# Kernel tuning notes

Measured on AMD Instinct MI355X. Metric: run time of the kernel, lower is better.

Reference implementation:

```python
import jax, jax.numpy as jnp
import numpy as np

BETA = 0.5

def setup_inputs() -> dict:
    key = jax.random.key(0)
    ks = jax.random.split(key, 12)
    B, H, d, hid = 2048, 100, 128, 256
    item_num, region_num, dist_num = 100000, 1000, 16
    return {
        "history": jax.random.randint(ks[0], (B, H), 0, item_num),
        "target": jax.random.randint(ks[1], (B,), 0, item_num),
        "history_region": jax.random.randint(ks[2], (B, H), 0, region_num),
        "target_region": jax.random.randint(ks[3], (B,), 0, region_num),
        "target_distance": jax.random.uniform(ks[4], (B,), dtype=jnp.float32),
        "E_hist": jax.random.normal(ks[5], (item_num, d), dtype=jnp.float32) * 0.01,
        "E_tgt": jax.random.normal(ks[6], (item_num, d), dtype=jnp.float32) * 0.01,
        "E_reg": jax.random.normal(ks[7], (region_num, d), dtype=jnp.float32) * 0.01,
        "E_dist": jax.random.normal(ks[8], (dist_num, d), dtype=jnp.float32) * 0.01,
        "W1": jax.random.normal(ks[9], (hid, 2 * d), dtype=jnp.float32) * 0.05,
        "b1": jnp.zeros((hid,), dtype=jnp.float32),
        "w2": jax.random.normal(ks[10], (hid,), dtype=jnp.float32) * 0.05,
    }

def reference(history, target, history_region, target_region, target_distance,
              E_hist, E_tgt, E_reg, E_dist, W1, b1, w2):
    # history embeddings: [B,H,2d]
    hist = jnp.concatenate([E_hist[history], E_reg[history_region]], axis=-1)
    # target embeddings: [B,1,2d]
    tgt = jnp.concatenate([E_tgt[target], E_reg[target_region]], axis=-1)[:, None, :]
    x = hist * tgt                                   # [B,H,2d]
    a = jax.nn.relu(jnp.einsum('bhd,kd->bhk', x, W1) + b1)  # [B,H,hid]
    score = jnp.einsum('bhk,k->bh', a, w2)           # [B,H]
    # distance bias: scalar per batch element
    dist = jnp.sum(target_distance[:, None] * E_dist[0], axis=1)  # [B]
    exp_A = jnp.exp(score + dist[:, None])           # [B,H]
    mask = (history != target[:, None]).astype(exp_A.dtype)
    exp_A = exp_A * mask
    exp_sum = jnp.power(jnp.sum(exp_A, axis=-1), BETA)  # [B]
    attn = exp_A / exp_sum[:, None]                  # [B,H]
    # weighted inner product: sum_h sum_d attn*hist*tgt
    pred = jnp.sum(hist * attn[:, :, None] * tgt, axis=(1, 2))  # [B]
    return jax.nn.sigmoid(pred)
```

## Files before the change

### kernel.cpp

```cpp
#include <hip/hip_runtime.h>
#include <stdint.h>

typedef __attribute__((ext_vector_type(8))) short bf16x8;
typedef __attribute__((ext_vector_type(4))) float f32x4;

#define HH  100
#define DD  128
#define HID 256

__device__ __forceinline__ unsigned short f2bf(float f) {
    unsigned int u = __float_as_uint(f);
    u += 0x7fffu + ((u >> 16) & 1u);
    return (unsigned short)(u >> 16);
}

__device__ __forceinline__ void load_lds_1k(const void* g, void* l) {
    __builtin_amdgcn_global_load_lds((const __attribute__((address_space(1))) unsigned int*)g,
                                     (__attribute__((address_space(3))) unsigned int*)l,
                                     16, 0, 0);
}

__global__ void w1_pack(const float* __restrict__ W1, unsigned short* __restrict__ W1p) {
    int unit = blockIdx.x * 256 + threadIdx.x;
    int lane = unit & 63;
    int s    = (unit >> 6) & 7;
    int st   = unit >> 9;
    int col  = lane & 15, quad = lane >> 4;
    const float* src = W1 + (size_t)(st * 16 + col) * HID + s * 32 + quad * 8;
    union { unsigned short u[8]; bf16x8 v; } o;
    #pragma unroll
    for (int j = 0; j < 8; j++) o.u[j] = f2bf(src[j]);
    *(bf16x8*)(W1p + (size_t)unit * 8) = o.v;
}

__global__ __launch_bounds__(512, 4) void nais_kernel(
    const int* __restrict__ history,
    const int* __restrict__ target,
    const int* __restrict__ history_region,
    const int* __restrict__ target_region,
    const float* __restrict__ target_distance,
    const float* __restrict__ E_hist,
    const float* __restrict__ E_tgt,
    const float* __restrict__ E_reg,
    const float* __restrict__ E_dist,
    const float* __restrict__ b1,
    const float* __restrict__ w2,
    const unsigned short* __restrict__ W1p,
    float* __restrict__ out)
{
    __shared__ __align__(16) unsigned short Bs[2][8192];
    __shared__ __align__(16) float tgts[HID];
    __shared__ __align__(16) float b1s[HID];
    __shared__ __align__(16) float w2s[HID];
    __shared__ float score[128];
    __shared__ float xsum[128];
    __shared__ float eA[HH];
    __shared__ float exs[HH];
    __shared__ int hidx[HH];
    __shared__ int hreg[HH];
    __shared__ float s_sumE;

    const int b    = blockIdx.x;
    const int t    = threadIdx.x;
    const int lane = t & 63;
    const int wave = t >> 6;
    const int col  = lane & 15;
    const int quad = lane >> 4;

    const int   tg    = target[b];
    const float tdist = target_distance[b];

    if (t < HH) {
        hidx[t] = history[b * HH + t];
        hreg[t] = history_region[b * HH + t];
    }
    if (wave == 4) {
        float4 v;
        if (lane < 32) v = *(const float4*)(E_tgt + (size_t)tg * DD + lane * 4);
        else           v = *(const float4*)(E_reg + (size_t)target_region[b] * DD + (lane - 32) * 4);
        *(float4*)(tgts + lane * 4) = v;
    }
    if (wave == 5) {
        *(float4*)(b1s + lane * 4) = *(const float4*)(b1 + lane * 4);
        *(float4*)(w2s + lane * 4) = *(const float4*)(w2 + lane * 4);
    }
    if (wave == 6) {
        float v = E_dist[lane] + E_dist[64 + lane];
        #pragma unroll
        for (int off = 32; off; off >>= 1) v += __shfl_xor(v, off);
        if (lane == 0) s_sumE = v;
    }
    __syncthreads();

    {
        const char* g = (const char*)W1p + wave * 2048 + lane * 16;
        char*       l = (char*)&Bs[0][0] + wave * 2048;
        load_lds_1k(g, l);
        load_lds_1k(g + 1024, l + 1024);
    }

    const int row = wave * 16 + col;
    const int rc  = (row < HH) ? row : row - 64;
    const int ih  = hidx[rc];
    const int ir  = hreg[rc];
    const float* ph = E_hist + (size_t)ih * DD + quad * 8;
    const float* pr = E_reg  + (size_t)ir * DD + quad * 8;
    bf16x8 afrag[8];
    float acc = 0.f;
    #pragma unroll
    for (int c = 0; c < 2; c++) {
        #pragma unroll
        for (int si = 0; si < 4; si++) {
            const int s = c * 4 + si;
            const float* src = (s < 4) ? (ph + s * 32) : (pr + (s - 4) * 32);
            float4 v0 = *(const float4*)src;
            float4 v1 = *(const float4*)(src + 4);
            const float* tp = tgts + s * 32 + quad * 8;
            float4 t0 = *(const float4*)tp, t1 = *(const float4*)(tp + 4);
            float x0 = v0.x * t0.x, x1 = v0.y * t0.y, x2 = v0.z * t0.z, x3 = v0.w * t0.w;
            float x4 = v1.x * t1.x, x5 = v1.y * t1.y, x6 = v1.z * t1.z, x7 = v1.w * t1.w;
            acc += (x0 + x1) + (x2 + x3) + ((x4 + x5) + (x6 + x7));
            union { unsigned short u[8]; bf16x8 v; } fb;
            fb.u[0] = f2bf(x0); fb.u[1] = f2bf(x1); fb.u[2] = f2bf(x2); fb.u[3] = f2bf(x3);
            fb.u[4] = f2bf(x4); fb.u[5] = f2bf(x5); fb.u[6] = f2bf(x6); fb.u[7] = f2bf(x7);
            afrag[s] = fb.v;
        }
        asm volatile("" ::: "memory");
    }
    {
        float v = acc;
        v += __shfl_xor(v, 16);
        v += __shfl_xor(v, 32);
        if (quad == 0) xsum[row] = v;
    }

    float sacc[4] = {};
    #pragma unroll 1
    for (int k = 0; k < 8; k++) {
        __syncthreads();
        if (k < 7) {
            const char* g = (const char*)W1p + (k + 1) * 16384 + wave * 2048 + lane * 16;
            char*       l = (char*)&Bs[(k + 1) & 1][0] + wave * 2048;
            load_lds_1k(g, l);
            load_lds_1k(g + 1024, l + 1024);
        }
        const unsigned short* buf = &Bs[k & 1][0];
        #pragma unroll
        for (int sti = 0; sti < 2; sti++) {
            const int st = k * 2 + sti;
            const float bb = b1s[st * 16 + col];
            const float ww = w2s[st * 16 + col];
            f32x4 acc0 = {0.f, 0.f, 0.f, 0.f};
            #pragma unroll
            for (int s = 0; s < 8; s++) {
                bf16x8 bfrag = *(const bf16x8*)(buf + ((sti * 8 + s) * 64 + lane) * 8);
                acc0 = __builtin_amdgcn_mfma_f32_16x16x32_bf16(afrag[s], bfrag, acc0, 0, 0, 0);
            }
            #pragma unroll
            for (int r = 0; r < 4; r++) {
                float z = acc0[r] + bb;
                sacc[r] += (z > 0.f) ? z * ww : 0.f;
            }
        }
    }
    #pragma unroll
    for (int r = 0; r < 4; r++) {
        float z = sacc[r];
        z += __shfl_xor(z, 1);
        z += __shfl_xor(z, 2);
        z += __shfl_xor(z, 4);
        z += __shfl_xor(z, 8);
        sacc[r] = z;
    }
    if (col == 0) {
        #pragma unroll
        for (int r = 0; r < 4; r++)
            score[wave * 16 + quad * 4 + r] = sacc[r];
    }

    __syncthreads();

    const float dist = tdist * s_sumE;
    if (t < HH) {
        float e = (hidx[t] != tg) ? expf(score[t] + dist) : 0.f;
        eA[t]  = e;
        exs[t] = e * xsum[t];
    }
    __syncthreads();
    if (t < 64) {
        float s1 = eA[t]  + ((t + 64 < HH) ? eA[t + 64]  : 0.f);
        float s2 = exs[t] + ((t + 64 < HH) ? exs[t + 64] : 0.f);
        #pragma unroll
        for (int off = 32; off; off >>= 1) {
            s1 += __shfl_xor(s1, off);
            s2 += __shfl_xor(s2, off);
        }
        if (t == 0) {
            float pred = s2 / sqrtf(s1);
            out[b] = 1.f / (1.f + expf(-pred));
        }
    }
}

extern "C" void kernel_launch(void* const* d_in, const int* in_sizes, int n_in,
                              void* d_out, int out_size, void* d_ws, size_t ws_size,
                              hipStream_t stream) {
    const int*   history         = (const int*)d_in[0];
    const int*   target          = (const int*)d_in[1];
    const int*   history_region  = (const int*)d_in[2];
    const int*   target_region   = (const int*)d_in[3];
    const float* target_distance = (const float*)d_in[4];
    const float* E_hist          = (const float*)d_in[5];
    const float* E_tgt           = (const float*)d_in[6];
    const float* E_reg           = (const float*)d_in[7];
    const float* E_dist          = (const float*)d_in[8];
    const float* W1              = (const float*)d_in[9];
    const float* b1              = (const float*)d_in[10];
    const float* w2              = (const float*)d_in[11];

    unsigned short* W1p = (unsigned short*)d_ws;
    const int B = in_sizes[1];

    w1_pack<<<32, 256, 0, stream>>>(W1, W1p);
    nais_kernel<<<B, 512, 0, stream>>>(history, target, history_region, target_region,
                                       target_distance, E_hist, E_tgt, E_reg, E_dist,
                                       b1, w2, W1p, (float*)d_out);
}
```

Baseline: 192.6 us.

## Switch MFMA to 32x32x16 tiles with 4 waves per block

Replaces the 16x16x32 bf16 MFMA tiling (8 waves of 16 rows) with 32x32x16 MFMA (4 waves of 32 rows), repacking W1 to match the new B-fragment layout and halving the block to 256 threads. Each wave now holds 16 A fragments and a 16-wide accumulator, and does more work per LDS-loaded B fragment. The intent is fewer MFMA issues and fewer LDS reads per output, and less redundant padded-row work. In exchange each wave uses more registers and the launch-bounds occupancy target is lower.

After: 198.1 us. 1.03x slower.

```diff
diff --git a/kernel.cpp b/kernel.cpp
--- a/kernel.cpp
+++ b/kernel.cpp
@@ -2,7 +2,7 @@
 #include <stdint.h>
 
 typedef __attribute__((ext_vector_type(8))) short bf16x8;
-typedef __attribute__((ext_vector_type(4))) float f32x4;
+typedef __attribute__((ext_vector_type(16))) float f32x16;
 
 #define HH  100
 #define DD  128
@@ -23,17 +23,18 @@
 __global__ void w1_pack(const float* __restrict__ W1, unsigned short* __restrict__ W1p) {
     int unit = blockIdx.x * 256 + threadIdx.x;
     int lane = unit & 63;
-    int s    = (unit >> 6) & 7;
-    int st   = unit >> 9;
-    int col  = lane & 15, quad = lane >> 4;
-    const float* src = W1 + (size_t)(st * 16 + col) * HID + s * 32 + quad * 8;
+    int s    = (unit >> 6) & 15;
+    int st   = unit >> 10;
+    int n    = st * 32 + (lane & 31);
+    int k    = s * 16 + (lane >> 5) * 8;
+    const float* src = W1 + (size_t)n * HID + k;
     union { unsigned short u[8]; bf16x8 v; } o;
     #pragma unroll
     for (int j = 0; j < 8; j++) o.u[j] = f2bf(src[j]);
     *(bf16x8*)(W1p + (size_t)unit * 8) = o.v;
 }
 
-__global__ __launch_bounds__(512, 4) void nais_kernel(
+__global__ __launch_bounds__(256, 2) void nais_kernel(
     const int* __restrict__ history,
     const int* __restrict__ target,
     const int* __restrict__ history_region,
@@ -64,8 +65,8 @@
     const int t    = threadIdx.x;
     const int lane = t & 63;
     const int wave = t >> 6;
-    const int col  = lane & 15;
-    const int quad = lane >> 4;
+    const int m32  = lane & 31;
+    const int half = lane >> 5;
 
     const int   tg    = target[b];
     const float tdist = target_distance[b];
@@ -74,48 +75,48 @@
         hidx[t] = history[b * HH + t];
         hreg[t] = history_region[b * HH + t];
     }
-    if (wave == 4) {
+    if (wave == 1) {
+        float v = E_dist[lane] + E_dist[64 + lane];
+        #pragma unroll
+        for (int off = 32; off; off >>= 1) v += __shfl_xor(v, off);
+        if (lane == 0) s_sumE = v;
+    }
+    if (wave == 2) {
         float4 v;
         if (lane < 32) v = *(const float4*)(E_tgt + (size_t)tg * DD + lane * 4);
         else           v = *(const float4*)(E_reg + (size_t)target_region[b] * DD + (lane - 32) * 4);
         *(float4*)(tgts + lane * 4) = v;
     }
-    if (wave == 5) {
+    if (wave == 3) {
         *(float4*)(b1s + lane * 4) = *(const float4*)(b1 + lane * 4);
         *(float4*)(w2s + lane * 4) = *(const float4*)(w2 + lane * 4);
     }
-    if (wave == 6) {
-        float v = E_dist[lane] + E_dist[64 + lane];
-        #pragma unroll
-        for (int off = 32; off; off >>= 1) v += __shfl_xor(v, off);
-        if (lane == 0) s_sumE = v;
-    }
     __syncthreads();
 
     {
-        const char* g = (const char*)W1p + wave * 2048 + lane * 16;
-        char*       l = (char*)&Bs[0][0] + wave * 2048;
-        load_lds_1k(g, l);
-        load_lds_1k(g + 1024, l + 1024);
-    }
-
-    const int row = wave * 16 + col;
+        const char* g = (const char*)W1p + wave * 4096 + lane * 16;
+        char*       l = (char*)&Bs[0][0] + wave * 4096;
+        #pragma unroll
+        for (int i = 0; i < 4; i++) load_lds_1k(g + i * 1024, l + i * 1024);
+    }
+
+    const int row = wave * 32 + m32;
     const int rc  = (row < HH) ? row : row - 64;
     const int ih  = hidx[rc];
     const int ir  = hreg[rc];
-    const float* ph = E_hist + (size_t)ih * DD + quad * 8;
-    const float* pr = E_reg  + (size_t)ir * DD + quad * 8;
-    bf16x8 afrag[8];
+    const float* ph = E_hist + (size_t)ih * DD + half * 8;
+    const float* pr = E_reg  + (size_t)ir * DD + half * 8;
+    bf16x8 afrag[16];
     float acc = 0.f;
     #pragma unroll
-    for (int c = 0; c < 2; c++) {
+    for (int c = 0; c < 4; c++) {
         #pragma unroll
         for (int si = 0; si < 4; si++) {
             const int s = c * 4 + si;
-            const float* src = (s < 4) ? (ph + s * 32) : (pr + (s - 4) * 32);
+            const float* src = (s < 8) ? (ph + s * 16) : (pr + (s - 8) * 16);
             float4 v0 = *(const float4*)src;
             float4 v1 = *(const float4*)(src + 4);
-            const float* tp = tgts + s * 32 + quad * 8;
+            const float* tp = tgts + s * 16 + half * 8;
             float4 t0 = *(const float4*)tp, t1 = *(const float4*)(tp + 4);
             float x0 = v0.x * t0.x, x1 = v0.y * t0.y, x2 = v0.z * t0.z, x3 = v0.w * t0.w;
             float x4 = v1.x * t1.x, x5 = v1.y * t1.y, x6 = v1.z * t1.z, x7 = v1.w * t1.w;
@@ -129,53 +130,49 @@
     }
     {
         float v = acc;
-        v += __shfl_xor(v, 16);
         v += __shfl_xor(v, 32);
-        if (quad == 0) xsum[row] = v;
-    }
-
-    float sacc[4] = {};
+        if (half == 0) xsum[row] = v;
+    }
+
+    float sacc[16] = {};
     #pragma unroll 1
     for (int k = 0; k < 8; k++) {
         __syncthreads();
         if (k < 7) {
-            const char* g = (const char*)W1p + (k + 1) * 16384 + wave * 2048 + lane * 16;
-            char*       l = (char*)&Bs[(k + 1) & 1][0] + wave * 2048;
-            load_lds_1k(g, l);
-            load_lds_1k(g + 1024, l + 1024);
+            const char* g = (const char*)W1p + (k + 1) * 16384 + wave * 4096 + lane * 16;
+            char*       l = (char*)&Bs[(k + 1) & 1][0] + wave * 4096;
+            #pragma unroll
+            for (int i = 0; i < 4; i++) load_lds_1k(g + i * 1024, l + i * 1024);
         }
         const unsigned short* buf = &Bs[k & 1][0];
-        #pragma unroll
-        for (int sti = 0; sti < 2; sti++) {
-            const int st = k * 2 + sti;
-            const float bb = b1s[st * 16 + col];
-            const float ww = w2s[st * 16 + col];
-            f32x4 acc0 = {0.f, 0.f, 0.f, 0.f};
-            #pragma unroll
-            for (int s = 0; s < 8; s++) {
-                bf16x8 bfrag = *(const bf16x8*)(buf + ((sti * 8 + s) * 64 + lane) * 8);
-                acc0 = __builtin_amdgcn_mfma_f32_16x16x32_bf16(afrag[s], bfrag, acc0, 0, 0, 0);
-            }
-            #pragma unroll
-            for (int r = 0; r < 4; r++) {
-                float z = acc0[r] + bb;
-                sacc[r] += (z > 0.f) ? z * ww : 0.f;
-            }
+        f32x16 acc0 = {};
+        #pragma unroll
+        for (int s = 0; s < 16; s++) {
+            bf16x8 bfrag = *(const bf16x8*)(buf + (s * 64 + lane) * 8);
+            acc0 = __builtin_amdgcn_mfma_f32_32x32x16_bf16(afrag[s], bfrag, acc0, 0, 0, 0);
+        }
+        const float bb = b1s[k * 32 + m32];
+        const float ww = w2s[k * 32 + m32];
+        #pragma unroll
+        for (int r = 0; r < 16; r++) {
+            float z = acc0[r] + bb;
+            sacc[r] += (z > 0.f) ? z * ww : 0.f;
         }
     }
     #pragma unroll
-    for (int r = 0; r < 4; r++) {
+    for (int r = 0; r < 16; r++) {
         float z = sacc[r];
         z += __shfl_xor(z, 1);
         z += __shfl_xor(z, 2);
         z += __shfl_xor(z, 4);
         z += __shfl_xor(z, 8);
+        z += __shfl_xor(z, 16);
         sacc[r] = z;
     }
-    if (col == 0) {
-        #pragma unroll
-        for (int r = 0; r < 4; r++)
-            score[wave * 16 + quad * 4 + r] = sacc[r];
+    if (m32 == 0) {
+        #pragma unroll
+        for (int r = 0; r < 16; r++)
+            score[wave * 32 + (r & 3) + 8 * (r >> 2) + 4 * half] = sacc[r];
     }
 
     __syncthreads();
@@ -222,7 +219,7 @@
     const int B = in_sizes[1];
 
     w1_pack<<<32, 256, 0, stream>>>(W1, W1p);
-    nais_kernel<<<B, 512, 0, stream>>>(history, target, history_region, target_region,
+    nais_kernel<<<B, 256, 0, stream>>>(history, target, history_region, target_region,
                                        target_distance, E_hist, E_tgt, E_reg, E_dist,
                                        b1, w2, W1p, (float*)d_out);
 }
```
